# Performance work log

Hardware: AMD Instinct MI355X
Metric: run time of the kernel (lower is better)

## Reference

```python
import jax, jax.numpy as jnp
import numpy as np

D_MODEL = 1024
N_HEADS = 16
HEAD_DIM = D_MODEL // N_HEADS  # 64


def setup_inputs() -> dict:
    key = jax.random.key(0)
    ks = jax.random.split(key, 6)
    scale_in = 1.0 / np.sqrt(D_MODEL)
    scale_hd = 1.0 / np.sqrt(N_HEADS * HEAD_DIM)
    inputs_q = jax.random.normal(ks[0], (4, 2048, D_MODEL), dtype=jnp.float32)
    # DenseGeneral kernels: [d_model, n_heads, head_dim] for q/k/v, [n_heads, head_dim, d_model] for out.
    Wq = jax.random.normal(ks[1], (D_MODEL, N_HEADS, HEAD_DIM), dtype=jnp.float32) * scale_in
    Wk = jax.random.normal(ks[2], (D_MODEL, N_HEADS, HEAD_DIM), dtype=jnp.float32) * scale_in
    Wv = jax.random.normal(ks[3], (D_MODEL, N_HEADS, HEAD_DIM), dtype=jnp.float32) * scale_in
    Wo = jax.random.normal(ks[4], (N_HEADS, HEAD_DIM, D_MODEL), dtype=jnp.float32) * scale_hd
    bq = jnp.zeros((N_HEADS, HEAD_DIM), dtype=jnp.float32)
    bk = jnp.zeros((N_HEADS, HEAD_DIM), dtype=jnp.float32)
    bv = jnp.zeros((N_HEADS, HEAD_DIM), dtype=jnp.float32)
    bo = jnp.zeros((D_MODEL,), dtype=jnp.float32)
    return {"inputs_q": inputs_q, "Wq": Wq, "bq": bq, "Wk": Wk, "bk": bk,
            "Wv": Wv, "bv": bv, "Wo": Wo, "bo": bo}


def reference(inputs_q, Wq, bq, Wk, bk, Wv, bv, Wo, bo):
    # Self-attention: inputs_kv = inputs_q.
    # QKV projections (DenseGeneral axis=-1 -> (heads, head_dim)).
    q = jnp.einsum('bsf,fhd->bshd', inputs_q, Wq) + bq  # [B,S,H,D]
    k = jnp.einsum('bsf,fhd->bshd', inputs_q, Wk) + bk
    v = jnp.einsum('bsf,fhd->bshd', inputs_q, Wv) + bv
    # Scaled dot-product attention (naive: full [B,H,S,S] scores, as in source).
    q = q / jnp.sqrt(jnp.asarray(HEAD_DIM, dtype=q.dtype))
    scores = jnp.einsum('bqhd,bkhd->bhqk', q, k)  # [B,H,Sq,Sk]
    attn = jax.nn.softmax(scores, axis=-1)
    x = jnp.einsum('bhqk,bkhd->bqhd', attn, v)  # [B,S,H,D]
    # Output projection over (heads, head_dim).
    out = jnp.einsum('bqhd,hdf->bqf', x, Wo) + bo  # [B,S,d_model]
    return out
```

## Files before the change

kernel.cpp:

```cpp
#include <hip/hip_runtime.h>
#include <math.h>

typedef __bf16 bf16;
typedef __attribute__((ext_vector_type(4))) __bf16 bf16x4;
typedef __attribute__((ext_vector_type(8))) __bf16 bf16x8;
typedef __attribute__((ext_vector_type(4))) float f32x4;

#define LOG2E 1.44269504088896340736f

__device__ __forceinline__ f32x4 mfma16(bf16x8 a, bf16x8 b, f32x4 c) {
  return __builtin_amdgcn_mfma_f32_16x16x32_bf16(a, b, c, 0, 0, 0);
}

__device__ __forceinline__ void load_lds16(const bf16* g, bf16* l) {
  __builtin_amdgcn_global_load_lds(
      (__attribute__((address_space(1))) void*)(g),
      (__attribute__((address_space(3))) void*)(l), 16, 0, 0);
}

__global__ __launch_bounds__(256) void cvt_x(const float* __restrict__ x,
                                             bf16* __restrict__ xb) {
  int i = (blockIdx.x * 256 + threadIdx.x) * 8;
  float4 a = *(const float4*)&x[i];
  float4 b = *(const float4*)&x[i + 4];
  bf16x8 v;
  v[0] = (bf16)a.x; v[1] = (bf16)a.y; v[2] = (bf16)a.z; v[3] = (bf16)a.w;
  v[4] = (bf16)b.x; v[5] = (bf16)b.y; v[6] = (bf16)b.z; v[7] = (bf16)b.w;
  *(bf16x8*)&xb[i] = v;
}

__global__ __launch_bounds__(256) void wtrans(
    const float* __restrict__ Wq, const float* __restrict__ Wk,
    const float* __restrict__ Wv, const float* __restrict__ Wo,
    bf16* __restrict__ Wcat, bf16* __restrict__ WoT, float qscale) {
  __shared__ float t[32][33];
  const int z = blockIdx.z;
  const float* src = (z == 0) ? Wq : (z == 1) ? Wk : (z == 2) ? Wv : Wo;
  bf16* dst = (z == 3) ? WoT : (Wcat + (size_t)z * 1024 * 1024);
  const float scale = (z == 0) ? qscale : 1.0f;
  int c0 = blockIdx.x * 32, r0 = blockIdx.y * 32;
  for (int i = threadIdx.y; i < 32; i += 8)
    t[i][threadIdx.x] = src[(r0 + i) * 1024 + c0 + threadIdx.x];
  __syncthreads();
  for (int i = threadIdx.y; i < 32; i += 8)
    dst[(c0 + i) * 1024 + r0 + threadIdx.x] = (bf16)(t[threadIdx.x][i] * scale);
}

__global__ __launch_bounds__(256) void vtrans(const bf16* __restrict__ Vs,
                                              bf16* __restrict__ Vt) {
  __shared__ bf16 t[64][72];
  const int bh = blockIdx.y;
  const int s0 = blockIdx.x * 64;
  const size_t base = (size_t)bh * 2048 * 64;
  const int tid = threadIdx.x;
  {
    int r = tid >> 3, c = (tid & 7) * 8;
    *(uint4*)&t[r][c]      = *(const uint4*)&Vs[base + (size_t)(s0 + r) * 64 + c];
    *(uint4*)&t[r + 32][c] = *(const uint4*)&Vs[base + (size_t)(s0 + r + 32) * 64 + c];
  }
  __syncthreads();
  int d = tid >> 2, sc = (tid & 3) * 16;
  bf16 tmp[16];
#pragma unroll
  for (int k = 0; k < 16; k++) tmp[k] = t[sc + k][d];
  *(uint4*)&Vt[base + (size_t)d * 2048 + s0 + sc]     = *(uint4*)&tmp[0];
  *(uint4*)&Vt[base + (size_t)d * 2048 + s0 + sc + 8] = *(uint4*)&tmp[8];
}

template <int MODE>
__global__ __launch_bounds__(256, 2) void gemm_bt(
    const bf16* __restrict__ A, const bf16* __restrict__ Bt, int N, int K,
    bf16* __restrict__ Qo, bf16* __restrict__ Ko, bf16* __restrict__ Vo,
    const float* __restrict__ b0, const float* __restrict__ b1,
    const float* __restrict__ b2,
    float* __restrict__ Co, const float* __restrict__ bias) {
  __shared__ bf16 lA[128 * 32];
  __shared__ bf16 lB[128 * 32];
  const int tid = threadIdx.x;
  const int lane = tid & 63, w = tid >> 6;
  const int l16 = lane & 15, quad = lane >> 4;
  const int swz = (l16 >> 2) & 3;
  const int wm = w >> 1, wn = w & 1;
  const int id = blockIdx.x;
  const int xcd = id & 7, local = id >> 3;
  const int m0 = (xcd * 8 + (local & 7)) * 128;
  const int n0 = (local >> 3) * 128;

  const int srow = w * 16 + (lane >> 2);
  const int scol = (((lane & 3) ^ ((lane >> 4) & 3)) * 8);
  const bf16* Ag = A + (size_t)(m0 + srow) * K + scol;
  const bf16* Bg = Bt + (size_t)(n0 + srow) * K + scol;
  bf16* lAw = &lA[w * 16 * 32];
  bf16* lBw = &lB[w * 16 * 32];

  f32x4 acc[4][4] = {};
  for (int k0 = 0; k0 < K; k0 += 32) {
    __syncthreads();
    load_lds16(Ag + k0, lAw);
    load_lds16(Ag + k0 + (size_t)64 * K, lAw + 64 * 32);
    load_lds16(Bg + k0, lBw);
    load_lds16(Bg + k0 + (size_t)64 * K, lBw + 64 * 32);
    __syncthreads();
    bf16x8 af[4], bfr[4];
#pragma unroll
    for (int i = 0; i < 4; i++)
      af[i] = *(const bf16x8*)&lA[(wm * 64 + i * 16 + l16) * 32 + (quad ^ swz) * 8];
#pragma unroll
    for (int i = 0; i < 4; i++)
      bfr[i] = *(const bf16x8*)&lB[(wn * 64 + i * 16 + l16) * 32 + (quad ^ swz) * 8];
#pragma unroll
    for (int i = 0; i < 4; i++)
#pragma unroll
      for (int j = 0; j < 4; j++)
        acc[i][j] = mfma16(af[i], bfr[j], acc[i][j]);
  }

  if (MODE == 0) {
    const int which = n0 >> 10;
    bf16* dst = (which == 0) ? Qo : (which == 1) ? Ko : Vo;
    const float* bsrc = (which == 0) ? b0 : (which == 1) ? b1 : b2;
    const float bscale = (which == 0) ? (0.125f * LOG2E) : 1.0f;
#pragma unroll
    for (int j = 0; j < 4; j++) {
      const int nn = (n0 & 1023) + wn * 64 + j * 16 + l16;
      const int h = nn >> 6, d = nn & 63;
      const float bias_v = bsrc[nn] * bscale;
#pragma unroll
      for (int i = 0; i < 4; i++) {
#pragma unroll
        for (int rg = 0; rg < 4; rg++) {
          const int grow = m0 + wm * 64 + i * 16 + quad * 4 + rg;
          const int bb = grow >> 11, s = grow & 2047;
          dst[((size_t)(bb * 16 + h) * 2048 + s) * 64 + d] =
              (bf16)(acc[i][j][rg] + bias_v);
        }
      }
    }
  } else {
#pragma unroll
    for (int j = 0; j < 4; j++) {
      const int gcol = n0 + wn * 64 + j * 16 + l16;
      const float bias_v = bias[gcol];
#pragma unroll
      for (int i = 0; i < 4; i++) {
#pragma unroll
        for (int rg = 0; rg < 4; rg++) {
          const int grow = m0 + wm * 64 + i * 16 + quad * 4 + rg;
          Co[(size_t)grow * N + gcol] = acc[i][j][rg] + bias_v;
        }
      }
    }
  }
}

__global__ __launch_bounds__(256, 2) void attn(const bf16* __restrict__ Q,
                                               const bf16* __restrict__ Kb,
                                               const bf16* __restrict__ Vt,
                                               bf16* __restrict__ X2) {
  __shared__ bf16 lK[2][2][64][32];
  __shared__ bf16 lV[2][2][64][32];
  __shared__ bf16 lP[4][64][72];
  const int tid = threadIdx.x;
  const int lane = tid & 63, w = tid >> 6;
  const int l16 = lane & 15, quad = lane >> 4;
  const int swz = (l16 >> 2) & 3;
  const int bh = blockIdx.x & 63;
  const int q0 = (blockIdx.x >> 6) * 256;
  const int bb = bh >> 4, h = bh & 15;
  const size_t base = (size_t)bh * 2048 * 64;

  bf16x8 aq[4][2];
#pragma unroll
  for (int mi = 0; mi < 4; mi++)
#pragma unroll
    for (int kh = 0; kh < 2; kh++)
      aq[mi][kh] = *(const bf16x8*)&Q[base + (size_t)(q0 + w * 64 + mi * 16 + l16) * 64 + kh * 32 + quad * 8];

  f32x4 o_acc[4][4] = {};
  float l_r[4] = {0.f, 0.f, 0.f, 0.f};

  const int drow = lane >> 2;
  const int dcol = (((lane & 3) ^ ((lane >> 4) & 3)) * 8);
  const bf16* Kg = Kb + base + (size_t)(w * 16 + drow) * 64 + dcol;
  const bf16* Vg = Vt + base + (size_t)(w * 16 + drow) * 2048 + dcol;

  load_lds16(Kg, &lK[0][0][w * 16][0]);
  load_lds16(Kg + 32, &lK[0][1][w * 16][0]);
  load_lds16(Vg, &lV[0][0][w * 16][0]);
  load_lds16(Vg + 32, &lV[0][1][w * 16][0]);

  for (int kt = 0; kt < 32; kt++) {
    const int p = kt & 1;
    __syncthreads();
    if (kt + 1 < 32) {
      const bf16* kg = Kg + (size_t)(kt + 1) * 64 * 64;
      const bf16* vg = Vg + (kt + 1) * 64;
      load_lds16(kg, &lK[p ^ 1][0][w * 16][0]);
      load_lds16(kg + 32, &lK[p ^ 1][1][w * 16][0]);
      load_lds16(vg, &lV[p ^ 1][0][w * 16][0]);
      load_lds16(vg + 32, &lV[p ^ 1][1][w * 16][0]);
    }

#pragma unroll
    for (int g = 0; g < 2; g++) {
      f32x4 s[2][4] = {};
#pragma unroll
      for (int n2 = 0; n2 < 2; n2++) {
        const int ni = g * 2 + n2;
        bf16x8 ak0 = *(const bf16x8*)&lK[p][0][ni * 16 + l16][(quad ^ swz) * 8];
        bf16x8 ak1 = *(const bf16x8*)&lK[p][1][ni * 16 + l16][(quad ^ swz) * 8];
#pragma unroll
        for (int mi = 0; mi < 4; mi++) {
          s[n2][mi] = mfma16(ak0, aq[mi][0], s[n2][mi]);
          s[n2][mi] = mfma16(ak1, aq[mi][1], s[n2][mi]);
        }
      }
#pragma unroll
      for (int n2 = 0; n2 < 2; n2++) {
        const int ni = g * 2 + n2;
#pragma unroll
        for (int mi = 0; mi < 4; mi++) {
          bf16x4 pw;
          float lp = 0.f;
#pragma unroll
          for (int rg = 0; rg < 4; rg++) {
            float pv = __builtin_amdgcn_exp2f(s[n2][mi][rg]);
            lp += pv;
            pw[rg] = (bf16)pv;
          }
          l_r[mi] += lp;
          *(bf16x4*)&lP[w][mi * 16 + l16][ni * 16 + quad * 4] = pw;
        }
      }
    }

    bf16x8 vf0[4], vf1[4];
#pragma unroll
    for (int di = 0; di < 4; di++) {
      vf0[di] = *(const bf16x8*)&lV[p][0][di * 16 + l16][(quad ^ swz) * 8];
      vf1[di] = *(const bf16x8*)&lV[p][1][di * 16 + l16][(quad ^ swz) * 8];
    }
#pragma unroll
    for (int mi = 0; mi < 4; mi++) {
      bf16x8 ap0 = *(const bf16x8*)&lP[w][mi * 16 + l16][quad * 8];
      bf16x8 ap1 = *(const bf16x8*)&lP[w][mi * 16 + l16][32 + quad * 8];
#pragma unroll
      for (int di = 0; di < 4; di++) {
        o_acc[mi][di] = mfma16(ap0, vf0[di], o_acc[mi][di]);
        o_acc[mi][di] = mfma16(ap1, vf1[di], o_acc[mi][di]);
      }
    }
  }

#pragma unroll
  for (int mi = 0; mi < 4; mi++) {
    float l = l_r[mi];
    l += __shfl_xor(l, 16);
    l += __shfl_xor(l, 32);
    l_r[mi] = 1.f / l;
  }
#pragma unroll
  for (int mi = 0; mi < 4; mi++)
#pragma unroll
    for (int rg = 0; rg < 4; rg++) {
      float inv = __shfl(l_r[mi], quad * 4 + rg);
      int s = q0 + w * 64 + mi * 16 + quad * 4 + rg;
#pragma unroll
      for (int di = 0; di < 4; di++) {
        float v = o_acc[mi][di][rg] * inv;
        X2[((size_t)bb * 2048 + s) * 1024 + h * 64 + di * 16 + l16] = (bf16)v;
      }
    }
}

extern "C" void kernel_launch(void* const* d_in, const int* in_sizes, int n_in,
                              void* d_out, int out_size, void* d_ws, size_t ws_size,
                              hipStream_t stream) {
  const float* x  = (const float*)d_in[0];
  const float* Wq = (const float*)d_in[1];
  const float* bq = (const float*)d_in[2];
  const float* Wk = (const float*)d_in[3];
  const float* bk = (const float*)d_in[4];
  const float* Wv = (const float*)d_in[5];
  const float* bv = (const float*)d_in[6];
  const float* Wo = (const float*)d_in[7];
  const float* bo = (const float*)d_in[8];
  float* out = (float*)d_out;

  char* ws = (char*)d_ws;
  bf16* Xb   = (bf16*)(ws);
  bf16* Wcat = (bf16*)(ws + 16777216);
  bf16* WoT  = (bf16*)(ws + 23068672);
  bf16* Qb   = (bf16*)(ws + 25165824);
  bf16* Kbf  = (bf16*)(ws + 41943040);
  bf16* Vt   = (bf16*)(ws + 58720256);
  bf16* Vs   = (bf16*)d_out;
  bf16* X2   = Xb;

  cvt_x<<<4096, 256, 0, stream>>>(x, Xb);
  wtrans<<<dim3(32, 32, 4), dim3(32, 8), 0, stream>>>(
      Wq, Wk, Wv, Wo, Wcat, WoT, 0.125f * LOG2E);

  gemm_bt<0><<<1536, 256, 0, stream>>>(Xb, Wcat, 3072, 1024,
      Qb, Kbf, Vs, bq, bk, bv, nullptr, nullptr);

  vtrans<<<dim3(32, 64), 256, 0, stream>>>(Vs, Vt);

  attn<<<512, 256, 0, stream>>>(Qb, Kbf, Vt, X2);

  gemm_bt<1><<<512, 256, 0, stream>>>(X2, WoT, 1024, 1024,
      nullptr, nullptr, nullptr, nullptr, nullptr, nullptr, out, bo);
}
```

Measured before the change: 279.4 us.

## Fuse input prep kernels and write V transposed directly from QKV GEMM

Merges the x-to-bf16 conversion and weight transpose kernels into one launch using an extra grid z-slice. The QKV GEMM epilogue now writes V straight into the transposed [bh, d, s] layout, which removes the separate vtrans kernel and its round trip through global memory. The cost is launch overhead saved against strided, poorly coalesced scalar stores for the V portion of the epilogue.

Result: slower. 289.4 us (+3.6%).

```diff
diff --git a/kernel.cpp b/kernel.cpp
--- a/kernel.cpp
+++ b/kernel.cpp
@@ -18,53 +18,39 @@
       (__attribute__((address_space(3))) void*)(l), 16, 0, 0);
 }
 
-__global__ __launch_bounds__(256) void cvt_x(const float* __restrict__ x,
-                                             bf16* __restrict__ xb) {
-  int i = (blockIdx.x * 256 + threadIdx.x) * 8;
-  float4 a = *(const float4*)&x[i];
-  float4 b = *(const float4*)&x[i + 4];
-  bf16x8 v;
-  v[0] = (bf16)a.x; v[1] = (bf16)a.y; v[2] = (bf16)a.z; v[3] = (bf16)a.w;
-  v[4] = (bf16)b.x; v[5] = (bf16)b.y; v[6] = (bf16)b.z; v[7] = (bf16)b.w;
-  *(bf16x8*)&xb[i] = v;
-}
-
-__global__ __launch_bounds__(256) void wtrans(
-    const float* __restrict__ Wq, const float* __restrict__ Wk,
-    const float* __restrict__ Wv, const float* __restrict__ Wo,
+__global__ __launch_bounds__(256) void prep(
+    const float* __restrict__ x, const float* __restrict__ Wq,
+    const float* __restrict__ Wk, const float* __restrict__ Wv,
+    const float* __restrict__ Wo, bf16* __restrict__ xb,
     bf16* __restrict__ Wcat, bf16* __restrict__ WoT, float qscale) {
   __shared__ float t[32][33];
   const int z = blockIdx.z;
-  const float* src = (z == 0) ? Wq : (z == 1) ? Wk : (z == 2) ? Wv : Wo;
-  bf16* dst = (z == 3) ? WoT : (Wcat + (size_t)z * 1024 * 1024);
-  const float scale = (z == 0) ? qscale : 1.0f;
-  int c0 = blockIdx.x * 32, r0 = blockIdx.y * 32;
-  for (int i = threadIdx.y; i < 32; i += 8)
-    t[i][threadIdx.x] = src[(r0 + i) * 1024 + c0 + threadIdx.x];
-  __syncthreads();
-  for (int i = threadIdx.y; i < 32; i += 8)
-    dst[(c0 + i) * 1024 + r0 + threadIdx.x] = (bf16)(t[threadIdx.x][i] * scale);
-}
-
-__global__ __launch_bounds__(256) void vtrans(const bf16* __restrict__ Vs,
-                                              bf16* __restrict__ Vt) {
-  __shared__ bf16 t[64][72];
-  const int bh = blockIdx.y;
-  const int s0 = blockIdx.x * 64;
-  const size_t base = (size_t)bh * 2048 * 64;
   const int tid = threadIdx.x;
-  {
-    int r = tid >> 3, c = (tid & 7) * 8;
-    *(uint4*)&t[r][c]      = *(const uint4*)&Vs[base + (size_t)(s0 + r) * 64 + c];
-    *(uint4*)&t[r + 32][c] = *(const uint4*)&Vs[base + (size_t)(s0 + r + 32) * 64 + c];
-  }
-  __syncthreads();
-  int d = tid >> 2, sc = (tid & 3) * 16;
-  bf16 tmp[16];
-#pragma unroll
-  for (int k = 0; k < 16; k++) tmp[k] = t[sc + k][d];
-  *(uint4*)&Vt[base + (size_t)d * 2048 + s0 + sc]     = *(uint4*)&tmp[0];
-  *(uint4*)&Vt[base + (size_t)d * 2048 + s0 + sc + 8] = *(uint4*)&tmp[8];
+  if (z == 4) {
+    const int blk = blockIdx.y * 32 + blockIdx.x;
+    const int base = blk * 8192;
+#pragma unroll
+    for (int u = 0; u < 4; u++) {
+      int i = base + u * 2048 + tid * 8;
+      float4 a = *(const float4*)&x[i];
+      float4 b = *(const float4*)&x[i + 4];
+      bf16x8 v;
+      v[0] = (bf16)a.x; v[1] = (bf16)a.y; v[2] = (bf16)a.z; v[3] = (bf16)a.w;
+      v[4] = (bf16)b.x; v[5] = (bf16)b.y; v[6] = (bf16)b.z; v[7] = (bf16)b.w;
+      *(bf16x8*)&xb[i] = v;
+    }
+  } else {
+    const float* src = (z == 0) ? Wq : (z == 1) ? Wk : (z == 2) ? Wv : Wo;
+    bf16* dst = (z == 3) ? WoT : (Wcat + (size_t)z * 1024 * 1024);
+    const float scale = (z == 0) ? qscale : 1.0f;
+    const int tx = tid & 31, ty = tid >> 5;
+    int c0 = blockIdx.x * 32, r0 = blockIdx.y * 32;
+    for (int i = ty; i < 32; i += 8)
+      t[i][tx] = src[(r0 + i) * 1024 + c0 + tx];
+    __syncthreads();
+    for (int i = ty; i < 32; i += 8)
+      dst[(c0 + i) * 1024 + r0 + tx] = (bf16)(t[tx][i] * scale);
+  }
 }
 
 template <int MODE>
@@ -120,6 +106,8 @@
     bf16* dst = (which == 0) ? Qo : (which == 1) ? Ko : Vo;
     const float* bsrc = (which == 0) ? b0 : (which == 1) ? b1 : b2;
     const float bscale = (which == 0) ? (0.125f * LOG2E) : 1.0f;
+    const int ss = (which == 2) ? 1 : 64;
+    const int sd = (which == 2) ? 2048 : 1;
 #pragma unroll
     for (int j = 0; j < 4; j++) {
       const int nn = (n0 & 1023) + wn * 64 + j * 16 + l16;
@@ -131,7 +119,7 @@
         for (int rg = 0; rg < 4; rg++) {
           const int grow = m0 + wm * 64 + i * 16 + quad * 4 + rg;
           const int bb = grow >> 11, s = grow & 2047;
-          dst[((size_t)(bb * 16 + h) * 2048 + s) * 64 + d] =
+          dst[(size_t)(bb * 16 + h) * 131072 + (size_t)s * ss + d * sd] =
               (bf16)(acc[i][j][rg] + bias_v);
         }
       }
@@ -294,17 +282,13 @@
   bf16* Qb   = (bf16*)(ws + 25165824);
   bf16* Kbf  = (bf16*)(ws + 41943040);
   bf16* Vt   = (bf16*)(ws + 58720256);
-  bf16* Vs   = (bf16*)d_out;
   bf16* X2   = Xb;
 
-  cvt_x<<<4096, 256, 0, stream>>>(x, Xb);
-  wtrans<<<dim3(32, 32, 4), dim3(32, 8), 0, stream>>>(
-      Wq, Wk, Wv, Wo, Wcat, WoT, 0.125f * LOG2E);
+  prep<<<dim3(32, 32, 5), 256, 0, stream>>>(
+      x, Wq, Wk, Wv, Wo, Xb, Wcat, WoT, 0.125f * LOG2E);
 
   gemm_bt<0><<<1536, 256, 0, stream>>>(Xb, Wcat, 3072, 1024,
-      Qb, Kbf, Vs, bq, bk, bv, nullptr, nullptr);
-
-  vtrans<<<dim3(32, 64), 256, 0, stream>>>(Vs, Vt);
+      Qb, Kbf, Vt, bq, bk, bv, nullptr, nullptr);
 
   attn<<<512, 256, 0, stream>>>(Qb, Kbf, Vt, X2);
 
```
